# Kernel tuning notes

Measured on AMD Instinct MI355X. Metric: run time of the kernel, lower is better.

The kernel has to match this reference:

```python
import jax, jax.numpy as jnp
import numpy as np

B, C, H, W = 32, 64, 128, 128
RADIUS = 30


def _dw(x, w, dil, pad):
    # depthwise conv, NCHW, groups = C
    return jax.lax.conv_general_dilated(
        x, w, window_strides=(1, 1), padding=[(pad, pad), (pad, pad)],
        rhs_dilation=(dil, dil),
        dimension_numbers=('NCHW', 'OIHW', 'NCHW'),
        feature_group_count=x.shape[1])


def _pw(x, w):
    # 1x1 conv: w is [out_ch, in_ch]
    return jnp.einsum('bchw,oc->bohw', x, w)


def _aff(x, s, b):
    # folded BatchNorm (inference): per-channel scale + bias
    return x * s[None, :, None, None] + b[None, :, None, None]


def setup_inputs() -> dict:
    key = jax.random.key(0)
    ks = iter(jax.random.split(key, 40))
    nk = lambda: next(ks)
    rn = lambda shape, sc=0.1: jax.random.normal(nk(), shape, jnp.float32) * sc
    ru = lambda shape: jax.random.uniform(nk(), shape, jnp.float32, minval=0.5, maxval=1.5)
    d = {'x': jax.random.normal(nk(), (B, C, H, W), jnp.float32)}
    d['dws_dw'] = rn((C, 1, 3, 3)); d['dws_s1'] = ru((C,)); d['dws_b1'] = rn((C,))
    d['dws_pw'] = rn((C, C)); d['dws_s2'] = ru((C,)); d['dws_b2'] = rn((C,))
    kern = {1: 1, 2: 3, 3: 3, 4: 3}
    for i in (1, 2, 3, 4):
        d[f'dw{i}_w'] = rn((C, 1, kern[i], kern[i]))
        d[f'dw{i}_s'] = ru((C,)); d[f'dw{i}_b'] = rn((C,))
        d[f'pw{i}_w'] = rn((C // 4, C)); d[f'pw{i}_s'] = ru((C // 4,)); d[f'pw{i}_b'] = rn((C // 4,))
    d['conv_w'] = rn((1, C)); d['conv_s'] = ru((1,)); d['conv_b'] = rn((1,))
    d['radius'] = RADIUS
    return d


def reference(x, dws_dw, dws_s1, dws_b1, dws_pw, dws_s2, dws_b2,
              dw1_w, dw1_s, dw1_b, pw1_w, pw1_s, pw1_b,
              dw2_w, dw2_s, dw2_b, pw2_w, pw2_s, pw2_b,
              dw3_w, dw3_s, dw3_b, pw3_w, pw3_s, pw3_b,
              dw4_w, dw4_s, dw4_b, pw4_w, pw4_s, pw4_b,
              conv_w, conv_s, conv_b, radius):
    rows, cols = x.shape[-2], x.shape[-1]
    # vectorized radial mask (original builds this with a Python double loop)
    ii = jnp.arange(rows, dtype=jnp.float32)[:, None]
    jj = jnp.arange(cols, dtype=jnp.float32)[None, :]
    dis = jnp.sqrt((ii - rows / 2) ** 2 + (jj - rows / 2) ** 2)  # note: imageSize=rows for both axes, as in original
    mask = (dis < radius).astype(x.dtype)
    # FFT high-pass filter
    xf = jnp.fft.fftshift(jnp.fft.fft2(x, axes=(-2, -1)), axes=(-2, -1))
    hf = xf * (1.0 - mask)
    x_h = jnp.abs(jnp.fft.ifft2(jnp.fft.ifftshift(hf, axes=(-2, -1)), axes=(-2, -1))).astype(x.dtype)
    # DWSConv: depthwise 3x3 + BN + ReLU, then pointwise + BN + ReLU
    e = jax.nn.relu(_aff(_dw(x_h, dws_dw, 1, 1), dws_s1, dws_b1))
    e = jax.nn.relu(_aff(_pw(e, dws_pw), dws_s2, dws_b2))
    skip = e

    def branch(t, dw_w, dw_s, dw_b, pw_w, pw_s, pw_b, dil, pad):
        # DWConv (depthwise + BN + ReLU) then BasicConv2d 1x1 (conv + BN)
        t = jax.nn.relu(_aff(_dw(t, dw_w, dil, pad), dw_s, dw_b))
        return _aff(_pw(t, pw_w), pw_s, pw_b)

    em = jnp.concatenate([
        branch(e, dw1_w, dw1_s, dw1_b, pw1_w, pw1_s, pw1_b, 1, 0),
        branch(e, dw2_w, dw2_s, dw2_b, pw2_w, pw2_s, pw2_b, 1, 1),
        branch(e, dw3_w, dw3_s, dw3_b, pw3_w, pw3_s, pw3_b, 3, 3),
        branch(e, dw4_w, dw4_s, dw4_b, pw4_w, pw4_s, pw4_b, 5, 5),
    ], axis=1) + skip
    edge = jax.nn.relu(_aff(_pw(em, conv_w), conv_s, conv_b))  # [B,1,H,W]
    return _aff(_pw(x + edge, conv_w), conv_s, conv_b)  # shared self.conv applied again
```

## Files before the change

### kernel.cpp

```cpp
#include <hip/hip_runtime.h>


__device__ __forceinline__ float2 cmul(float2 a, float2 b) {
  return make_float2(a.x * b.x - a.y * b.y, a.x * b.y + a.y * b.x);
}
__device__ __forceinline__ float2 cadd(float2 a, float2 b) {
  return make_float2(a.x + b.x, a.y + b.y);
}
__device__ __forceinline__ float2 csub(float2 a, float2 b) {
  return make_float2(a.x - b.x, a.y - b.y);
}
__device__ __forceinline__ float2 conjf2(float2 a) {
  return make_float2(a.x, -a.y);
}

__device__ __forceinline__ void gload16(const float* g, void* l) {
  __builtin_amdgcn_global_load_lds(
      (const __attribute__((address_space(1))) void*)g,
      (__attribute__((address_space(3))) void*)l, 16, 0, 0);
}

__device__ __forceinline__ int swz(int r, int c) {
  return (r << 7) | ((c ^ (c >> 4)) ^ (r & 31));
}

__device__ __forceinline__ void bf3_fwd(float2 x[8], float2 t0, float2 t1,
                                        float2 t2, float2 t3, float2 tp0,
                                        float2 tp1, float2 tpp) {
  float2 y0 = cadd(x[0], x[4]), y4 = cmul(csub(x[0], x[4]), t0);
  float2 y1 = cadd(x[1], x[5]), y5 = cmul(csub(x[1], x[5]), t1);
  float2 y2 = cadd(x[2], x[6]), y6 = cmul(csub(x[2], x[6]), t2);
  float2 y3 = cadd(x[3], x[7]), y7 = cmul(csub(x[3], x[7]), t3);
  float2 z0 = cadd(y0, y2), z2 = cmul(csub(y0, y2), tp0);
  float2 z1 = cadd(y1, y3), z3 = cmul(csub(y1, y3), tp1);
  float2 z4 = cadd(y4, y6), z6 = cmul(csub(y4, y6), tp0);
  float2 z5 = cadd(y5, y7), z7 = cmul(csub(y5, y7), tp1);
  x[0] = cadd(z0, z1); x[1] = cmul(csub(z0, z1), tpp);
  x[2] = cadd(z2, z3); x[3] = cmul(csub(z2, z3), tpp);
  x[4] = cadd(z4, z5); x[5] = cmul(csub(z4, z5), tpp);
  x[6] = cadd(z6, z7); x[7] = cmul(csub(z6, z7), tpp);
}

__device__ __forceinline__ void bf3_inv(float2 x[8], float2 w0, float2 w10,
                                        float2 w11, float2 w20, float2 w21,
                                        float2 w22, float2 w23) {
  float2 t;
  t = cmul(x[1], w0); float2 y0 = cadd(x[0], t), y1 = csub(x[0], t);
  t = cmul(x[3], w0); float2 y2 = cadd(x[2], t), y3 = csub(x[2], t);
  t = cmul(x[5], w0); float2 y4 = cadd(x[4], t), y5 = csub(x[4], t);
  t = cmul(x[7], w0); float2 y6 = cadd(x[6], t), y7 = csub(x[6], t);
  t = cmul(y2, w10); float2 z0 = cadd(y0, t), z2 = csub(y0, t);
  t = cmul(y3, w11); float2 z1 = cadd(y1, t), z3 = csub(y1, t);
  t = cmul(y6, w10); float2 z4 = cadd(y4, t), z6 = csub(y4, t);
  t = cmul(y7, w11); float2 z5 = cadd(y5, t), z7 = csub(y5, t);
  t = cmul(z4, w20); x[0] = cadd(z0, t); x[4] = csub(z0, t);
  t = cmul(z5, w21); x[1] = cadd(z1, t); x[5] = csub(z1, t);
  t = cmul(z6, w22); x[2] = cadd(z2, t); x[6] = csub(z2, t);
  t = cmul(z7, w23); x[3] = cadd(z3, t); x[7] = csub(z3, t);
}

template <bool COL, int S>
__device__ __forceinline__ void fwd_tri(float2* img, const float2* tw,
                                        int tid) {
  constexpr int m4 = 1 << (S - 2);
#pragma unroll
  for (int k = 0; k < 2; ++k) {
    int g = tid + (k << 10);
    int line = COL ? (g & 127) : (g >> 4);
    int gidx = COL ? (g >> 7) : (g & 15);
    int q = gidx >> (S - 2);
    int j = gidx & (m4 - 1);
    int off0 = (q << (S + 1)) + j;
    int ad[8];
    float2 x[8];
#pragma unroll
    for (int i = 0; i < 8; ++i) {
      int el = off0 + i * m4;
      ad[i] = COL ? swz(el, line) : swz(line, el);
      x[i] = img[ad[i]];
    }
    bf3_fwd(x, tw[j << (6 - S)], tw[(j + m4) << (6 - S)],
            tw[(j + 2 * m4) << (6 - S)], tw[(j + 3 * m4) << (6 - S)],
            tw[j << (7 - S)], tw[(j + m4) << (7 - S)], tw[j << (8 - S)]);
#pragma unroll
    for (int i = 0; i < 8; ++i) img[ad[i]] = x[i];
  }
  __syncthreads();
}

__device__ __forceinline__ void fwd_rows6_g(const float* __restrict__ p0,
                                            const float* __restrict__ p1,
                                            float2* img, const float2* tw,
                                            int tid) {
#pragma unroll
  for (int k = 0; k < 2; ++k) {
    int g = tid + (k << 10);
    int line = g >> 4;
    int j = g & 15;
    float2 x[8];
#pragma unroll
    for (int i = 0; i < 8; ++i) {
      int a = (line << 7) + j + (i << 4);
      x[i] = make_float2(p0[a], p1[a]);
    }
    bf3_fwd(x, tw[j], tw[j + 16], tw[j + 32], tw[j + 48], tw[j << 1],
            tw[(j + 16) << 1], tw[j << 2]);
#pragma unroll
    for (int i = 0; i < 8; ++i) img[swz(line, j + (i << 4))] = x[i];
  }
  __syncthreads();
}

__device__ __forceinline__ void fwd_last_rows(float2* img, int tid) {
#pragma unroll
  for (int k = 0; k < 8; ++k) {
    int g = tid + (k << 10);
    int line = g >> 6;
    int pr = g & 63;
    int e0 = pr << 1;
    int a0 = swz(line, e0), a1 = swz(line, e0 + 1);
    float2 a = img[a0], b = img[a1];
    img[a0] = cadd(a, b);
    img[a1] = csub(a, b);
  }
  __syncthreads();
}

__device__ __forceinline__ void fwd_last_cols_mask(float2* img, int tid) {
#pragma unroll
  for (int k = 0; k < 8; ++k) {
    int g = tid + (k << 10);
    int line = g & 127;
    int pr = g >> 7;
    int e0 = pr << 1;
    int a0 = swz(e0, line), a1 = swz(e0 + 1, line);
    float2 a = img[a0], b = img[a1];
    float2 s = cadd(a, b), d = csub(a, b);
    int v = __brev((unsigned)line) >> 25;
    int dv = v - ((v >= 64) << 7);
    int u0 = __brev((unsigned)e0) >> 25;
    int du0 = u0 - ((u0 >= 64) << 7);
    int u1 = __brev((unsigned)(e0 + 1)) >> 25;
    int du1 = u1 - ((u1 >= 64) << 7);
    int dvv = dv * dv;
    img[a0] = (du0 * du0 + dvv < 900) ? make_float2(0.f, 0.f) : s;
    img[a1] = (du1 * du1 + dvv < 900) ? make_float2(0.f, 0.f) : d;
  }
  __syncthreads();
}

template <bool COL, int S>
__device__ __forceinline__ void inv_tri(float2* img, const float2* tw,
                                        int tid) {
  constexpr int m = 1 << S;
#pragma unroll
  for (int k = 0; k < 2; ++k) {
    int g = tid + (k << 10);
    int line = COL ? (g & 127) : (g >> 4);
    int gidx = COL ? (g >> 7) : (g & 15);
    int q = gidx >> S;
    int j = gidx & (m - 1);
    int off0 = (q << (S + 3)) + j;
    int ad[8];
    float2 x[8];
#pragma unroll
    for (int i = 0; i < 8; ++i) {
      int el = off0 + i * m;
      ad[i] = COL ? swz(el, line) : swz(line, el);
      x[i] = img[ad[i]];
    }
    bf3_inv(x, conjf2(tw[j << (6 - S)]), conjf2(tw[j << (5 - S)]),
            conjf2(tw[(j + m) << (5 - S)]), conjf2(tw[j << (4 - S)]),
            conjf2(tw[(j + m) << (4 - S)]), conjf2(tw[(j + 2 * m) << (4 - S)]),
            conjf2(tw[(j + 3 * m) << (4 - S)]));
#pragma unroll
    for (int i = 0; i < 8; ++i) img[ad[i]] = x[i];
  }
  __syncthreads();
}

__device__ __forceinline__ void inv_last_cols(float2* img, const float2* tw,
                                              int tid) {
#pragma unroll
  for (int k = 0; k < 8; ++k) {
    int g = tid + (k << 10);
    int line = g & 127;
    int j = g >> 7;
    int a0 = swz(j, line), a1 = swz(j + 64, line);
    float2 a = img[a0], b = img[a1];
    float2 t = cmul(b, conjf2(tw[j]));
    img[a0] = cadd(a, t);
    img[a1] = csub(a, t);
  }
  __syncthreads();
}

__device__ __forceinline__ void inv_last_rows_store(const float2* img,
                                                    const float2* tw,
                                                    float* __restrict__ q0,
                                                    float* __restrict__ q1,
                                                    int tid) {
#pragma unroll
  for (int k = 0; k < 8; ++k) {
    int g = tid + (k << 10);
    int line = g >> 6;
    int j = g & 63;
    float2 a = img[swz(line, j)], b = img[swz(line, j + 64)];
    float2 t = cmul(b, conjf2(tw[j]));
    float2 o0 = cadd(a, t), o1 = csub(a, t);
    int p = (line << 7) + j;
    q0[p] = fabsf(o0.x) * 6.103515625e-05f;
    q1[p] = fabsf(o0.y) * 6.103515625e-05f;
    q0[p + 64] = fabsf(o1.x) * 6.103515625e-05f;
    q1[p + 64] = fabsf(o1.y) * 6.103515625e-05f;
  }
}

__global__ __launch_bounds__(1024) void k_fft_hp(const float* __restrict__ x,
                                                 float* __restrict__ xh) {
  __shared__ float2 img[16384];
  __shared__ float2 tw[64];
  const int tid = threadIdx.x;
  const size_t base = (size_t)blockIdx.x * 32768;
  const float* p0 = x + base;
  const float* p1 = p0 + 16384;

  if (tid < 64) {
    float ang = -0.04908738521234052f * (float)tid;
    tw[tid] = make_float2(cosf(ang), sinf(ang));
  }
  __syncthreads();

  fwd_rows6_g(p0, p1, img, tw, tid);
  fwd_tri<false, 3>(img, tw, tid);
  fwd_last_rows(img, tid);
  fwd_tri<true, 6>(img, tw, tid);
  fwd_tri<true, 3>(img, tw, tid);
  fwd_last_cols_mask(img, tid);

  inv_tri<true, 0>(img, tw, tid);
  inv_tri<true, 3>(img, tw, tid);
  inv_last_cols(img, tw, tid);
  inv_tri<false, 0>(img, tw, tid);
  inv_tri<false, 3>(img, tw, tid);
  inv_last_rows_store(img, tw, xh + base, xh + base + 16384, tid);
}

#define DWS_G(chunk, buf)                                                      \
  {                                                                            \
    _Pragma("unroll") for (int k2 = 0; k2 < 4; ++k2) {                         \
      int idx = t + (k2 << 8);                                                 \
      if (idx < 800)                                                           \
        gload16(xh + xbase + (size_t)(chunk) * 131072 + offs[k2],              \
                &inT[buf][idx << 2]);                                          \
    }                                                                          \
  }

#define DWS_FIX(buf)                                                           \
  {                                                                            \
    _Pragma("unroll") for (int k2 = 0; k2 < 4; ++k2) {                         \
      if ((fixm >> k2) & 1)                                                    \
        *(float4*)&inT[buf][(t + (k2 << 8)) << 2] =                            \
            make_float4(0.f, 0.f, 0.f, 0.f);                                   \
    }                                                                          \
  }

__global__ __launch_bounds__(256) void k_dws(
    const float* __restrict__ xh, float* __restrict__ e,
    const float* __restrict__ dw_w, const float* __restrict__ s1,
    const float* __restrict__ b1, const float* __restrict__ pw_w,
    const float* __restrict__ s2, const float* __restrict__ b2) {
  __shared__ __align__(16) float inT[2][3200];

  const int t = threadIdx.x;
  const int L = ((blockIdx.x & 7) << 8) | (blockIdx.x >> 3);
  const int bb = L >> 6;
  const int ty = (L >> 2) & 15;
  const int tx = L & 3;
  const int r = t >> 5;
  const int x = t & 31;

  const int gy0 = (ty << 3) - 1;
  const int gxb = (tx << 5) - 4;
  const size_t xbase = (size_t)bb << 20;
  const bool bfix = (ty == 0) | (ty == 15) | (tx == 0) | (tx == 3);

  unsigned fixm = 0;
  int offs[4];
#pragma unroll
  for (int k2 = 0; k2 < 4; ++k2) {
    int idx = t + (k2 << 8);
    offs[k2] = 0;
    if (idx < 800) {
      int c = idx / 100;
      int rem = idx - c * 100;
      int row = rem / 10;
      int g = rem - row * 10;
      int grow = gy0 + row;
      int gcol = gxb + (g << 2);
      if ((grow < 0) | (grow > 127) | (gcol < 0) | (gcol > 124))
        fixm |= (1u << k2);
      int grc = grow < 0 ? 0 : (grow > 127 ? 127 : grow);
      int gcc = gcol < 0 ? 0 : (gcol > 124 ? 124 : gcol);
      offs[k2] = (c << 14) + (grc << 7) + gcc;
    }
  }

  float acc[64];
#pragma unroll
  for (int o = 0; o < 64; ++o) acc[o] = 0.f;

  DWS_G(0, 0);
  __syncthreads();

#pragma unroll 1
  for (int chunk = 0; chunk < 8; ++chunk) {
    if (bfix) {
      DWS_FIX(chunk & 1);
      __syncthreads();
    }
    if (chunk < 7) DWS_G(chunk + 1, (chunk + 1) & 1);
    const float* base = &inT[chunk & 1][0];

    float dwv[8];
#pragma unroll
    for (int c = 0; c < 8; ++c) {
      const int cg = (chunk << 3) + c;
      const float* wp = dw_w + cg * 9;
      const float* p = base + c * 400 + r * 40 + x + 3;
      float s = wp[0] * p[0];
      s = fmaf(wp[1], p[1], s);
      s = fmaf(wp[2], p[2], s);
      s = fmaf(wp[3], p[40], s);
      s = fmaf(wp[4], p[41], s);
      s = fmaf(wp[5], p[42], s);
      s = fmaf(wp[6], p[80], s);
      s = fmaf(wp[7], p[81], s);
      s = fmaf(wp[8], p[82], s);
      dwv[c] = fmaxf(fmaf(s, s1[cg], b1[cg]), 0.f);
    }

#pragma unroll
    for (int o = 0; o < 64; ++o) {
      const float* w = pw_w + (o << 6) + (chunk << 3);
#pragma unroll
      for (int c = 0; c < 8; ++c) acc[o] = fmaf(w[c], dwv[c], acc[o]);
    }
    __syncthreads();
  }

  const int gy = (ty << 3) + r;
  const int gx = (tx << 5) + x;
#pragma unroll
  for (int o = 0; o < 64; ++o) {
    float ev = fmaxf(fmaf(acc[o], s2[o], b2[o]), 0.f);
    e[(((size_t)bb * 64 + o) << 14) + (gy << 7) + gx] = ev;
  }
}

struct BrParams {
  const float *dw1w, *dw1s, *dw1b, *pw1w, *pw1s, *pw1b;
  const float *dw2w, *dw2s, *dw2b, *pw2w, *pw2s, *pw2b;
  const float *dw3w, *dw3s, *dw3b, *pw3w, *pw3s, *pw3b;
  const float *dw4w, *dw4s, *dw4b, *pw4w, *pw4s, *pw4b;
};

#define EDGE_G(chunk, buf)                                                     \
  {                                                                            \
    _Pragma("unroll") for (int k2 = 0; k2 < 9; ++k2) {                         \
      int idx = t + (k2 << 8);                                                 \
      if (idx < 2080) {                                                        \
        const float* src = eg + ebase + (size_t)(chunk) * 32768 + eoffs[k2];   \
        if ((fixm >> k2) & 1) src = zp;                  \
        gload16(src, &sE[buf][idx << 2]);                                      \
      }                                                                        \
    }                                                                          \
  }

__global__ __launch_bounds__(256) void k_edge_final(
    const float* __restrict__ eg, const float* __restrict__ xg,
    float* __restrict__ out, BrParams P, const float* __restrict__ cw,
    const float* __restrict__ cs, const float* __restrict__ cb,
    const float* __restrict__ zp) {
  __shared__ __align__(16) float sE[2][8320];
  __shared__ float w2r[768], w3r[768], w4r[768];
  __shared__ float chp[1024];
  __shared__ float dwSs[4][64], dwBs[4][64], gs[4][64];
  __shared__ float dw1Ws[64], cws[64];
  __shared__ float pss[4][16], pbs[4][16];
  __shared__ float KbS, swS;

  const int t = threadIdx.x;
  const int L = ((blockIdx.x & 7) << 5) | (blockIdx.x >> 3);
  const int bb = L >> 3;
  const int ty = L & 7;
  const int r = t >> 4;
  const int x0 = (t & 15) << 3;
  const int gy = (ty << 4) + r;
  const int gy0 = (ty << 4) - 5;
  const size_t ebase = (size_t)bb << 20;

  for (int i = t; i < 576; i += 256) {
    int row = i / 9, q = i - row * 9;
    w2r[row * 12 + q] = P.dw2w[i];
    w3r[row * 12 + q] = P.dw3w[i];
    w4r[row * 12 + q] = P.dw4w[i];
  }
  if (t < 64) {
    dw1Ws[t] = P.dw1w[t];
    cws[t] = cw[t];
    dwSs[0][t] = P.dw1s[t]; dwBs[0][t] = P.dw1b[t];
    dwSs[1][t] = P.dw2s[t]; dwBs[1][t] = P.dw2b[t];
    dwSs[2][t] = P.dw3s[t]; dwBs[2][t] = P.dw3b[t];
    dwSs[3][t] = P.dw4s[t]; dwBs[3][t] = P.dw4b[t];
  }
  if (t < 16) {
    pss[0][t] = P.pw1s[t]; pbs[0][t] = P.pw1b[t];
    pss[1][t] = P.pw2s[t]; pbs[1][t] = P.pw2b[t];
    pss[2][t] = P.pw3s[t]; pbs[2][t] = P.pw3b[t];
    pss[3][t] = P.pw4s[t]; pbs[3][t] = P.pw4b[t];
  }
  __syncthreads();
  {
    const int q = t >> 6, c = t & 63;
    const float* pwW = (q == 0) ? P.pw1w : (q == 1) ? P.pw2w
                        : (q == 2) ? P.pw3w : P.pw4w;
    float gv = 0.f;
#pragma unroll
    for (int o = 0; o < 16; ++o)
      gv = fmaf(cws[(q << 4) + o] * pss[q][o], pwW[(o << 6) + c], gv);
    gs[q][c] = gv;
  }
  if (t == 0) {
    float kb = 0.f, sw = 0.f;
#pragma unroll
    for (int i = 0; i < 64; ++i) {
      kb = fmaf(cws[i], pbs[i >> 4][i & 15], kb);
      sw += cws[i];
    }
    KbS = kb;
    swS = sw;
  }
  __syncthreads();
  if (t < 64) {
    float* cp = &chp[t << 4];
    cp[0] = dw1Ws[t];  cp[1] = cws[t];
    cp[2] = dwSs[0][t]; cp[3] = dwBs[0][t];
    cp[4] = dwSs[1][t]; cp[5] = dwBs[1][t];
    cp[6] = dwSs[2][t]; cp[7] = dwBs[2][t];
    cp[8] = dwSs[3][t]; cp[9] = dwBs[3][t];
    cp[10] = gs[0][t]; cp[11] = gs[1][t];
    cp[12] = gs[2][t]; cp[13] = gs[3][t];
  }

  unsigned fixm = 0;
  int eoffs[9];
#pragma unroll
  for (int k2 = 0; k2 < 9; ++k2) {
    int idx = t + (k2 << 8);
    eoffs[k2] = 0;
    if (idx < 2080) {
      int jj = idx >= 1040;
      int rem = idx - (jj ? 1040 : 0);
      int row = rem / 40;
      int q = rem - row * 40;
      int s = q ^ (q >> 3);
      int grow = gy0 + row;
      if ((grow < 0) | (grow > 127) | (s < 2) | (s > 33)) fixm |= (1u << k2);
      int grc = grow < 0 ? 0 : (grow > 127 ? 127 : grow);
      int sc = s < 2 ? 2 : (s > 33 ? 33 : s);
      eoffs[k2] = (jj << 14) + (grc << 7) + (sc << 2) - 8;
    }
  }

  const int gbase = (t & 15) << 1;
  int so[6];
#pragma unroll
  for (int k = 0; k < 6; ++k) {
    int g = gbase + k;
    so[k] = (g ^ (g >> 3)) << 2;
  }

  EDGE_G(0, 0);
  __syncthreads();

  float eacc[8], es8[8], sxa[8];
#pragma unroll
  for (int k = 0; k < 8; ++k) { eacc[k] = 0.f; es8[k] = 0.f; sxa[k] = 0.f; }

  const float csv = cs[0], cbv = cb[0];

#pragma unroll 1
  for (int c = 0; c < 32; ++c) {
    if (c + 1 < 32) EDGE_G(c + 1, (c + 1) & 1);
    const float* bp = &sE[c & 1][0];
#pragma unroll 1
    for (int j = 0; j < 2; ++j) {
      const int cg = (c << 1) + j;
      const float* ldc = bp + j * 4160;
      const float* xp = xg + (((size_t)bb * 64 + cg) << 14) + (gy << 7) + x0;
      float xv[8];
      *(float4*)&xv[0] = *(const float4*)xp;
      *(float4*)&xv[4] = *(const float4*)(xp + 4);
      const float4 Q0 = *(const float4*)&chp[cg << 4];
      const float4 Q1 = *(const float4*)&chp[(cg << 4) + 4];
      const float4 Q2 = *(const float4*)&chp[(cg << 4) + 8];
      const float4 Q3 = *(const float4*)&chp[(cg << 4) + 12];

      float cr[24];
      const float* rowc = ldc + (r + 5) * 160;
      *(float4*)&cr[0] = *(const float4*)(rowc + so[0]);
      *(float4*)&cr[4] = *(const float4*)(rowc + so[1]);
      *(float4*)&cr[8] = *(const float4*)(rowc + so[2]);
      *(float4*)&cr[12] = *(const float4*)(rowc + so[3]);
      *(float4*)&cr[16] = *(const float4*)(rowc + so[4]);
      *(float4*)&cr[20] = *(const float4*)(rowc + so[5]);

#pragma unroll
      for (int k = 0; k < 8; ++k) {
        float ec = cr[8 + k];
        es8[k] = fmaf(Q0.y, ec, es8[k]);
        float d0 = fmaxf(fmaf(ec * Q0.x, Q0.z, Q0.w), 0.f);
        eacc[k] = fmaf(Q2.z, d0, eacc[k]);
      }
      float mm[24], pp[24];
      {
        const float4 w2a = *(const float4*)&w2r[cg * 12];
        const float4 w2b = *(const float4*)&w2r[cg * 12 + 4];
        const float4 w2c = *(const float4*)&w2r[cg * 12 + 8];
        const float* rm = ldc + (r + 4) * 160;
        const float* rp = ldc + (r + 6) * 160;
        *(float4*)&mm[0] = *(const float4*)(rm + so[1]);
        *(float4*)&mm[4] = *(const float4*)(rm + so[2]);
        *(float4*)&mm[8] = *(const float4*)(rm + so[3]);
        *(float4*)&mm[12] = *(const float4*)(rm + so[4]);
        *(float4*)&pp[0] = *(const float4*)(rp + so[1]);
        *(float4*)&pp[4] = *(const float4*)(rp + so[2]);
        *(float4*)&pp[8] = *(const float4*)(rp + so[3]);
        *(float4*)&pp[12] = *(const float4*)(rp + so[4]);
#pragma unroll
        for (int k = 0; k < 8; ++k) {
          float s = w2a.x * mm[3 + k];
          s = fmaf(w2a.y, mm[4 + k], s);
          s = fmaf(w2a.z, mm[5 + k], s);
          s = fmaf(w2a.w, cr[7 + k], s);
          s = fmaf(w2b.x, cr[8 + k], s);
          s = fmaf(w2b.y, cr[9 + k], s);
          s = fmaf(w2b.z, pp[3 + k], s);
          s = fmaf(w2b.w, pp[4 + k], s);
          s = fmaf(w2c.x, pp[5 + k], s);
          float d1 = fmaxf(fmaf(s, Q1.x, Q1.y), 0.f);
          eacc[k] = fmaf(Q2.w, d1, eacc[k]);
        }
      }
      {
        const float4 w3a = *(const float4*)&w3r[cg * 12];
        const float4 w3b = *(const float4*)&w3r[cg * 12 + 4];
        const float4 w3c = *(const float4*)&w3r[cg * 12 + 8];
        const float* rm = ldc + (r + 2) * 160;
        const float* rp = ldc + (r + 8) * 160;
        *(float4*)&mm[0] = *(const float4*)(rm + so[1]);
        *(float4*)&mm[4] = *(const float4*)(rm + so[2]);
        *(float4*)&mm[8] = *(const float4*)(rm + so[3]);
        *(float4*)&mm[12] = *(const float4*)(rm + so[4]);
        *(float4*)&pp[0] = *(const float4*)(rp + so[1]);
        *(float4*)&pp[4] = *(const float4*)(rp + so[2]);
        *(float4*)&pp[8] = *(const float4*)(rp + so[3]);
        *(float4*)&pp[12] = *(const float4*)(rp + so[4]);
#pragma unroll
        for (int k = 0; k < 8; ++k) {
          float s = w3a.x * mm[1 + k];
          s = fmaf(w3a.y, mm[4 + k], s);
          s = fmaf(w3a.z, mm[7 + k], s);
          s = fmaf(w3a.w, cr[5 + k], s);
          s = fmaf(w3b.x, cr[8 + k], s);
          s = fmaf(w3b.y, cr[11 + k], s);
          s = fmaf(w3b.z, pp[1 + k], s);
          s = fmaf(w3b.w, pp[4 + k], s);
          s = fmaf(w3c.x, pp[7 + k], s);
          float d2 = fmaxf(fmaf(s, Q1.z, Q1.w), 0.f);
          eacc[k] = fmaf(Q3.x, d2, eacc[k]);
        }
      }
      {
        const float4 w4a = *(const float4*)&w4r[cg * 12];
        const float4 w4b = *(const float4*)&w4r[cg * 12 + 4];
        const float4 w4c = *(const float4*)&w4r[cg * 12 + 8];
        const float* rm = ldc + (r + 0) * 160;
        const float* rp = ldc + (r + 10) * 160;
        *(float4*)&mm[0] = *(const float4*)(rm + so[0]);
        *(float4*)&mm[4] = *(const float4*)(rm + so[1]);
        *(float4*)&mm[8] = *(const float4*)(rm + so[2]);
        *(float4*)&mm[12] = *(const float4*)(rm + so[3]);
        *(float4*)&mm[16] = *(const float4*)(rm + so[4]);
        *(float4*)&mm[20] = *(const float4*)(rm + so[5]);
        *(float4*)&pp[0] = *(const float4*)(rp + so[0]);
        *(float4*)&pp[4] = *(const float4*)(rp + so[1]);
        *(float4*)&pp[8] = *(const float4*)(rp + so[2]);
        *(float4*)&pp[12] = *(const float4*)(rp + so[3]);
        *(float4*)&pp[16] = *(const float4*)(rp + so[4]);
        *(float4*)&pp[20] = *(const float4*)(rp + so[5]);
#pragma unroll
        for (int k = 0; k < 8; ++k) {
          float s = w4a.x * mm[3 + k];
          s = fmaf(w4a.y, mm[8 + k], s);
          s = fmaf(w4a.z, mm[13 + k], s);
          s = fmaf(w4a.w, cr[3 + k], s);
          s = fmaf(w4b.x, cr[8 + k], s);
          s = fmaf(w4b.y, cr[13 + k], s);
          s = fmaf(w4b.z, pp[3 + k], s);
          s = fmaf(w4b.w, pp[8 + k], s);
          s = fmaf(w4c.x, pp[13 + k], s);
          float d3 = fmaxf(fmaf(s, Q2.x, Q2.y), 0.f);
          eacc[k] = fmaf(Q3.y, d3, eacc[k]);
        }
      }
#pragma unroll
      for (int k = 0; k < 8; ++k) sxa[k] = fmaf(Q0.y, xv[k], sxa[k]);
    }
    __syncthreads();
  }

  const float kb = KbS, sw = swS;
  float ov[8];
#pragma unroll
  for (int k = 0; k < 8; ++k) {
    float ee = fmaxf(fmaf(eacc[k] + kb + es8[k], csv, cbv), 0.f);
    ov[k] = fmaf(sxa[k] + ee * sw, csv, cbv);
  }
  float* op = out + ((size_t)bb << 14) + (gy << 7) + x0;
  *(float4*)op = *(float4*)&ov[0];
  *(float4*)(op + 4) = *(float4*)&ov[4];
}

extern "C" void kernel_launch(void* const* d_in, const int* in_sizes, int n_in,
                              void* d_out, int out_size, void* d_ws,
                              size_t ws_size, hipStream_t stream) {
  (void)in_sizes; (void)n_in; (void)out_size; (void)ws_size;
  const float* x = (const float*)d_in[0];
  const float* dws_dw = (const float*)d_in[1];
  const float* dws_s1 = (const float*)d_in[2];
  const float* dws_b1 = (const float*)d_in[3];
  const float* dws_pw = (const float*)d_in[4];
  const float* dws_s2 = (const float*)d_in[5];
  const float* dws_b2 = (const float*)d_in[6];
  BrParams P;
  P.dw1w = (const float*)d_in[7];  P.dw1s = (const float*)d_in[8];
  P.dw1b = (const float*)d_in[9];  P.pw1w = (const float*)d_in[10];
  P.pw1s = (const float*)d_in[11]; P.pw1b = (const float*)d_in[12];
  P.dw2w = (const float*)d_in[13]; P.dw2s = (const float*)d_in[14];
  P.dw2b = (const float*)d_in[15]; P.pw2w = (const float*)d_in[16];
  P.pw2s = (const float*)d_in[17]; P.pw2b = (const float*)d_in[18];
  P.dw3w = (const float*)d_in[19]; P.dw3s = (const float*)d_in[20];
  P.dw3b = (const float*)d_in[21]; P.pw3w = (const float*)d_in[22];
  P.pw3s = (const float*)d_in[23]; P.pw3b = (const float*)d_in[24];
  P.dw4w = (const float*)d_in[25]; P.dw4s = (const float*)d_in[26];
  P.dw4b = (const float*)d_in[27]; P.pw4w = (const float*)d_in[28];
  P.pw4s = (const float*)d_in[29]; P.pw4b = (const float*)d_in[30];
  const float* conv_w = (const float*)d_in[31];
  const float* conv_s = (const float*)d_in[32];
  const float* conv_b = (const float*)d_in[33];

  float* xh = (float*)d_ws;
  float* e = xh + (size_t)33554432;

  hipLaunchKernelGGL(k_fft_hp, dim3(1024), dim3(1024), 0, stream, x, xh);
  hipLaunchKernelGGL(k_dws, dim3(2048), dim3(256), 0, stream, xh, e, dws_dw,
                     dws_s1, dws_b1, dws_pw, dws_s2, dws_b2);
  hipMemsetAsync(xh, 0, 4096, stream);
  hipLaunchKernelGGL(k_edge_final, dim3(256), dim3(256), 0, stream, e, x,
                     (float*)d_out, P, conv_w, conv_s, conv_b,
                     (const float*)xh);
}
```

Before: 575.6 us.

## Restructure FFT high-pass into radix-16 plus radix-8 passes per dimension

Replaces the 128-point FFT decomposition (radix-8, radix-8, radix-2 passes per dimension) with one radix-16 register pass and one radix-8 pass per dimension, in both the forward and inverse transforms. The mask is fused into the final forward column pass, and the inverse magnitude store is fused into the last row pass. This cuts the number of shared-memory round trips and __syncthreads barriers in the FFT kernel. In exchange, each thread holds 16 complex values in registers, which raises register pressure at 1024 threads per block.

```diff
diff --git a/kernel.cpp b/kernel.cpp
--- a/kernel.cpp
+++ b/kernel.cpp
@@ -59,160 +59,87 @@
   t = cmul(z7, w23); x[3] = cadd(z3, t); x[7] = csub(z3, t);
 }
 
-template <bool COL, int S>
-__device__ __forceinline__ void fwd_tri(float2* img, const float2* tw,
-                                        int tid) {
-  constexpr int m4 = 1 << (S - 2);
-#pragma unroll
-  for (int k = 0; k < 2; ++k) {
-    int g = tid + (k << 10);
-    int line = COL ? (g & 127) : (g >> 4);
-    int gidx = COL ? (g >> 7) : (g & 15);
-    int q = gidx >> (S - 2);
-    int j = gidx & (m4 - 1);
-    int off0 = (q << (S + 1)) + j;
-    int ad[8];
-    float2 x[8];
-#pragma unroll
-    for (int i = 0; i < 8; ++i) {
-      int el = off0 + i * m4;
-      ad[i] = COL ? swz(el, line) : swz(line, el);
-      x[i] = img[ad[i]];
-    }
-    bf3_fwd(x, tw[j << (6 - S)], tw[(j + m4) << (6 - S)],
-            tw[(j + 2 * m4) << (6 - S)], tw[(j + 3 * m4) << (6 - S)],
-            tw[j << (7 - S)], tw[(j + m4) << (7 - S)], tw[j << (8 - S)]);
-#pragma unroll
-    for (int i = 0; i < 8; ++i) img[ad[i]] = x[i];
-  }
-  __syncthreads();
-}
-
-__device__ __forceinline__ void fwd_rows6_g(const float* __restrict__ p0,
-                                            const float* __restrict__ p1,
-                                            float2* img, const float2* tw,
-                                            int tid) {
-#pragma unroll
-  for (int k = 0; k < 2; ++k) {
-    int g = tid + (k << 10);
-    int line = g >> 4;
-    int j = g & 15;
-    float2 x[8];
-#pragma unroll
-    for (int i = 0; i < 8; ++i) {
-      int a = (line << 7) + j + (i << 4);
-      x[i] = make_float2(p0[a], p1[a]);
-    }
-    bf3_fwd(x, tw[j], tw[j + 16], tw[j + 32], tw[j + 48], tw[j << 1],
-            tw[(j + 16) << 1], tw[j << 2]);
-#pragma unroll
-    for (int i = 0; i < 8; ++i) img[swz(line, j + (i << 4))] = x[i];
-  }
-  __syncthreads();
-}
-
-__device__ __forceinline__ void fwd_last_rows(float2* img, int tid) {
-#pragma unroll
-  for (int k = 0; k < 8; ++k) {
-    int g = tid + (k << 10);
-    int line = g >> 6;
-    int pr = g & 63;
-    int e0 = pr << 1;
-    int a0 = swz(line, e0), a1 = swz(line, e0 + 1);
-    float2 a = img[a0], b = img[a1];
-    img[a0] = cadd(a, b);
-    img[a1] = csub(a, b);
-  }
-  __syncthreads();
-}
-
-__device__ __forceinline__ void fwd_last_cols_mask(float2* img, int tid) {
-#pragma unroll
-  for (int k = 0; k < 8; ++k) {
-    int g = tid + (k << 10);
-    int line = g & 127;
-    int pr = g >> 7;
-    int e0 = pr << 1;
-    int a0 = swz(e0, line), a1 = swz(e0 + 1, line);
-    float2 a = img[a0], b = img[a1];
-    float2 s = cadd(a, b), d = csub(a, b);
-    int v = __brev((unsigned)line) >> 25;
-    int dv = v - ((v >= 64) << 7);
-    int u0 = __brev((unsigned)e0) >> 25;
-    int du0 = u0 - ((u0 >= 64) << 7);
-    int u1 = __brev((unsigned)(e0 + 1)) >> 25;
-    int du1 = u1 - ((u1 >= 64) << 7);
-    int dvv = dv * dv;
-    img[a0] = (du0 * du0 + dvv < 900) ? make_float2(0.f, 0.f) : s;
-    img[a1] = (du1 * du1 + dvv < 900) ? make_float2(0.f, 0.f) : d;
-  }
-  __syncthreads();
-}
-
-template <bool COL, int S>
-__device__ __forceinline__ void inv_tri(float2* img, const float2* tw,
-                                        int tid) {
-  constexpr int m = 1 << S;
-#pragma unroll
-  for (int k = 0; k < 2; ++k) {
-    int g = tid + (k << 10);
-    int line = COL ? (g & 127) : (g >> 4);
-    int gidx = COL ? (g >> 7) : (g & 15);
-    int q = gidx >> S;
-    int j = gidx & (m - 1);
-    int off0 = (q << (S + 3)) + j;
-    int ad[8];
-    float2 x[8];
-#pragma unroll
-    for (int i = 0; i < 8; ++i) {
-      int el = off0 + i * m;
-      ad[i] = COL ? swz(el, line) : swz(line, el);
-      x[i] = img[ad[i]];
-    }
-    bf3_inv(x, conjf2(tw[j << (6 - S)]), conjf2(tw[j << (5 - S)]),
-            conjf2(tw[(j + m) << (5 - S)]), conjf2(tw[j << (4 - S)]),
-            conjf2(tw[(j + m) << (4 - S)]), conjf2(tw[(j + 2 * m) << (4 - S)]),
-            conjf2(tw[(j + 3 * m) << (4 - S)]));
-#pragma unroll
-    for (int i = 0; i < 8; ++i) img[ad[i]] = x[i];
-  }
-  __syncthreads();
-}
-
-__device__ __forceinline__ void inv_last_cols(float2* img, const float2* tw,
-                                              int tid) {
-#pragma unroll
-  for (int k = 0; k < 8; ++k) {
-    int g = tid + (k << 10);
-    int line = g & 127;
-    int j = g >> 7;
-    int a0 = swz(j, line), a1 = swz(j + 64, line);
-    float2 a = img[a0], b = img[a1];
-    float2 t = cmul(b, conjf2(tw[j]));
-    img[a0] = cadd(a, t);
-    img[a1] = csub(a, t);
-  }
-  __syncthreads();
-}
-
-__device__ __forceinline__ void inv_last_rows_store(const float2* img,
-                                                    const float2* tw,
-                                                    float* __restrict__ q0,
-                                                    float* __restrict__ q1,
-                                                    int tid) {
-#pragma unroll
-  for (int k = 0; k < 8; ++k) {
-    int g = tid + (k << 10);
-    int line = g >> 6;
-    int j = g & 63;
-    float2 a = img[swz(line, j)], b = img[swz(line, j + 64)];
-    float2 t = cmul(b, conjf2(tw[j]));
-    float2 o0 = cadd(a, t), o1 = csub(a, t);
-    int p = (line << 7) + j;
-    q0[p] = fabsf(o0.x) * 6.103515625e-05f;
-    q1[p] = fabsf(o0.y) * 6.103515625e-05f;
-    q0[p + 64] = fabsf(o1.x) * 6.103515625e-05f;
-    q1[p + 64] = fabsf(o1.y) * 6.103515625e-05f;
+__device__ __forceinline__ void bf4_fwd_b(float2 x[16], const float2* tw,
+                                          int b) {
+#pragma unroll
+  for (int i = 0; i < 8; ++i) {
+    float2 a = x[i], v = x[i + 8];
+    x[i] = cadd(a, v);
+    x[i + 8] = cmul(csub(a, v), tw[b + (i << 3)]);
+  }
+#pragma unroll
+  for (int h = 0; h < 16; h += 8)
+#pragma unroll
+    for (int i = 0; i < 4; ++i) {
+      float2 a = x[h + i], v = x[h + i + 4];
+      x[h + i] = cadd(a, v);
+      x[h + i + 4] = cmul(csub(a, v), tw[(b + (i << 3)) << 1]);
+    }
+#pragma unroll
+  for (int g = 0; g < 16; g += 4)
+#pragma unroll
+    for (int i = 0; i < 2; ++i) {
+      float2 a = x[g + i], v = x[g + i + 2];
+      x[g + i] = cadd(a, v);
+      x[g + i + 2] = cmul(csub(a, v), tw[(b + (i << 3)) << 2]);
+    }
+  float2 t3 = tw[b << 3];
+#pragma unroll
+  for (int p = 0; p < 16; p += 2) {
+    float2 a = x[p], v = x[p + 1];
+    x[p] = cadd(a, v);
+    x[p + 1] = cmul(csub(a, v), t3);
+  }
+}
+
+__device__ __forceinline__ void bf4_inv_c(float2 x[16], const float2* tw) {
+#pragma unroll
+  for (int p = 0; p < 16; p += 2) {
+    float2 a = x[p], b = x[p + 1];
+    x[p] = cadd(a, b);
+    x[p + 1] = csub(a, b);
+  }
+  float2 w32 = conjf2(tw[32]);
+#pragma unroll
+  for (int g = 0; g < 16; g += 4) {
+    {
+      float2 a = x[g], b = x[g + 2];
+      x[g] = cadd(a, b);
+      x[g + 2] = csub(a, b);
+    }
+    {
+      float2 t = cmul(x[g + 3], w32);
+      float2 a = x[g + 1];
+      x[g + 1] = cadd(a, t);
+      x[g + 3] = csub(a, t);
+    }
+  }
+#pragma unroll
+  for (int h = 0; h < 16; h += 8) {
+    {
+      float2 a = x[h], t = x[h + 4];
+      x[h] = cadd(a, t);
+      x[h + 4] = csub(a, t);
+    }
+#pragma unroll
+    for (int i = 1; i < 4; ++i) {
+      float2 t = cmul(x[h + i + 4], conjf2(tw[i << 4]));
+      float2 a = x[h + i];
+      x[h + i] = cadd(a, t);
+      x[h + i + 4] = csub(a, t);
+    }
+  }
+  {
+    float2 a = x[0], t = x[8];
+    x[0] = cadd(a, t);
+    x[8] = csub(a, t);
+  }
+#pragma unroll
+  for (int i = 1; i < 8; ++i) {
+    float2 t = cmul(x[i + 8], conjf2(tw[i << 3]));
+    float2 a = x[i];
+    x[i] = cadd(a, t);
+    x[i + 8] = csub(a, t);
   }
 }
 
@@ -231,19 +158,141 @@
   }
   __syncthreads();
 
-  fwd_rows6_g(p0, p1, img, tw, tid);
-  fwd_tri<false, 3>(img, tw, tid);
-  fwd_last_rows(img, tid);
-  fwd_tri<true, 6>(img, tw, tid);
-  fwd_tri<true, 3>(img, tw, tid);
-  fwd_last_cols_mask(img, tid);
-
-  inv_tri<true, 0>(img, tw, tid);
-  inv_tri<true, 3>(img, tw, tid);
-  inv_last_cols(img, tw, tid);
-  inv_tri<false, 0>(img, tw, tid);
-  inv_tri<false, 3>(img, tw, tid);
-  inv_last_rows_store(img, tw, xh + base, xh + base + 16384, tid);
+  float2 xr[16];
+
+  {
+    const int l = tid & 63, w = tid >> 6;
+    const int line = (l & 15) | ((w & 7) << 4);
+    const int b = (l >> 4) | ((w >> 3) << 2);
+#pragma unroll
+    for (int i = 0; i < 16; ++i) {
+      int a = (line << 7) + b + (i << 3);
+      xr[i] = make_float2(p0[a], p1[a]);
+    }
+    bf4_fwd_b(xr, tw, b);
+#pragma unroll
+    for (int i = 0; i < 16; ++i) img[swz(line, b + (i << 3))] = xr[i];
+  }
+  __syncthreads();
+
+#pragma unroll
+  for (int k = 0; k < 2; ++k) {
+    int g = tid + (k << 10);
+    int line = g >> 4;
+    int bs = (g & 15) << 3;
+    float2 x8[8];
+    int ad[8];
+#pragma unroll
+    for (int i = 0; i < 8; ++i) {
+      ad[i] = swz(line, bs + i);
+      x8[i] = img[ad[i]];
+    }
+    bf3_fwd(x8, tw[0], tw[16], tw[32], tw[48], tw[0], tw[32], tw[0]);
+#pragma unroll
+    for (int i = 0; i < 8; ++i) img[ad[i]] = x8[i];
+  }
+  __syncthreads();
+
+  {
+    const int col = tid & 127;
+    const int b = tid >> 7;
+#pragma unroll
+    for (int i = 0; i < 16; ++i) xr[i] = img[swz(b + (i << 3), col)];
+    bf4_fwd_b(xr, tw, b);
+#pragma unroll
+    for (int i = 0; i < 16; ++i) img[swz(b + (i << 3), col)] = xr[i];
+  }
+  __syncthreads();
+
+#pragma unroll
+  for (int k = 0; k < 2; ++k) {
+    int g = tid + (k << 10);
+    int col = g & 127;
+    int bs = (g >> 7) << 3;
+    float2 x8[8];
+    int ad[8];
+#pragma unroll
+    for (int i = 0; i < 8; ++i) {
+      ad[i] = swz(bs + i, col);
+      x8[i] = img[ad[i]];
+    }
+    bf3_fwd(x8, tw[0], tw[16], tw[32], tw[48], tw[0], tw[32], tw[0]);
+    int v = __brev((unsigned)col) >> 25;
+    int dv = v - ((v >= 64) << 7);
+    int dvv = dv * dv;
+#pragma unroll
+    for (int i = 0; i < 8; ++i) {
+      int u = __brev((unsigned)(bs + i)) >> 25;
+      int du = u - ((u >= 64) << 7);
+      img[ad[i]] = (du * du + dvv < 900) ? make_float2(0.f, 0.f) : x8[i];
+    }
+  }
+  __syncthreads();
+
+  {
+    const int col = tid & 127;
+    const int bs = (tid >> 7) << 4;
+#pragma unroll
+    for (int i = 0; i < 16; ++i) xr[i] = img[swz(bs + i, col)];
+    bf4_inv_c(xr, tw);
+#pragma unroll
+    for (int i = 0; i < 16; ++i) img[swz(bs + i, col)] = xr[i];
+  }
+  __syncthreads();
+
+#pragma unroll
+  for (int k = 0; k < 2; ++k) {
+    int g = tid + (k << 10);
+    int col = g & 127;
+    int j2 = g >> 7;
+    float2 x8[8];
+    int ad[8];
+#pragma unroll
+    for (int i = 0; i < 8; ++i) {
+      ad[i] = swz(j2 + (i << 4), col);
+      x8[i] = img[ad[i]];
+    }
+    bf3_inv(x8, conjf2(tw[j2 << 2]), conjf2(tw[j2 << 1]),
+            conjf2(tw[(j2 + 16) << 1]), conjf2(tw[j2]), conjf2(tw[j2 + 16]),
+            conjf2(tw[j2 + 32]), conjf2(tw[j2 + 48]));
+#pragma unroll
+    for (int i = 0; i < 8; ++i) img[ad[i]] = x8[i];
+  }
+  __syncthreads();
+
+  {
+    const int line = tid & 127;
+    const int bs = (tid >> 7) << 4;
+#pragma unroll
+    for (int i = 0; i < 16; ++i) xr[i] = img[swz(line, bs + i)];
+    bf4_inv_c(xr, tw);
+#pragma unroll
+    for (int i = 0; i < 16; ++i) img[swz(line, bs + i)] = xr[i];
+  }
+  __syncthreads();
+
+  {
+    float* q0 = xh + base;
+    float* q1 = q0 + 16384;
+#pragma unroll
+    for (int k = 0; k < 2; ++k) {
+      int g = tid + (k << 10);
+      int line = g >> 4;
+      int j2 = g & 15;
+      float2 x8[8];
+#pragma unroll
+      for (int i = 0; i < 8; ++i) x8[i] = img[swz(line, j2 + (i << 4))];
+      bf3_inv(x8, conjf2(tw[j2 << 2]), conjf2(tw[j2 << 1]),
+              conjf2(tw[(j2 + 16) << 1]), conjf2(tw[j2]), conjf2(tw[j2 + 16]),
+              conjf2(tw[j2 + 32]), conjf2(tw[j2 + 48]));
+#pragma unroll
+      for (int i = 0; i < 8; ++i) {
+        int p = (line << 7) + j2 + (i << 4);
+        q0[p] = fabsf(x8[i].x) * 6.103515625e-05f;
+        q1[p] = fabsf(x8[i].y) * 6.103515625e-05f;
+      }
+    }
+  }
 }
 
 #define DWS_G(chunk, buf)                                                      \
```

Result: slower. 594.6 us (+3.3%).
